# Optimization experiments

Measured on AMD Instinct MI355X. Metric: run time of the kernel, lower is better.

## Reference

```python
import jax, jax.numpy as jnp
import numpy as np

B, N, D, A = 2048, 32, 64, 8
MAX_ACTION = 1.0
VARIANCE = 1.0


def setup_inputs() -> dict:
    key = jax.random.key(0)
    k1, k2, k3, k4, k5 = jax.random.split(key, 5)
    mean = jax.random.normal(k1, (B, D), dtype=jnp.float32)
    # SPD covariance: small-scale L L^T + 0.1 I
    L = jax.random.normal(k2, (B, D, D), dtype=jnp.float32) * 0.05
    covariance = jnp.einsum('bij,bkj->bik', L, L) + 0.1 * jnp.eye(D, dtype=jnp.float32)
    centers = jax.random.normal(k3, (N, D), dtype=jnp.float32) * 0.5
    weights = jax.random.normal(k4, (N, A), dtype=jnp.float32) * 0.1
    lengthscales = jnp.ones((D,), dtype=jnp.float32) + 0.1 * jax.random.uniform(k5, (D,), dtype=jnp.float32)
    return {"mean": mean, "covariance": covariance, "centers": centers,
            "weights": weights, "lengthscales": lengthscales}


def squash_sin(mean, covariance, max_action):
    # mean: (B, K); covariance: (B, K, K)
    K = mean.shape[-1]
    ma = jnp.full((K,), max_action, dtype=mean.dtype)
    diag_cov = jnp.diagonal(covariance, axis1=-2, axis2=-1)          # (B, K)
    squashed_mean = ma * jnp.exp(-diag_cov / 2.0) * jnp.sin(mean)
    lq = -(diag_cov[..., :, None] + diag_cov[..., None, :]) / 2.0
    q = jnp.exp(lq)
    mean_diff = mean[..., :, None] - mean[..., None, :]
    mean_sum = mean[..., :, None] + mean[..., None, :]
    sq_cov = ((jnp.exp(lq + covariance) - q) * jnp.cos(mean_diff)
              - (jnp.exp(lq - covariance) - q) * jnp.cos(mean_sum))
    outer_max = ma[None, :] * ma[:, None]
    sq_cov = outer_max * sq_cov / 2.0
    # diag_embed of (B, K) -> (B, K, K)
    cross = (ma * jnp.exp(-diag_cov / 2.0) * jnp.cos(mean))[..., :, None] * jnp.eye(K, dtype=mean.dtype)
    return squashed_mean, sq_cov, cross


def reference(mean, covariance, centers, weights, lengthscales):
    b = mean.shape[0]
    inv_l = 1.0 / lengthscales                                        # (D,)
    # B_mat = diag(inv_l) @ cov @ diag(inv_l) + I  (B, D, D)
    B_mat = covariance * (inv_l[:, None] * inv_l[None, :]) + jnp.eye(D, dtype=mean.dtype)
    inp = centers[None, :, :] - mean[:, None, :]                      # (B, N, D)
    scaled_inp = inp * inv_l                                          # (B, N, D)
    t = jnp.swapaxes(jnp.linalg.solve(B_mat, jnp.swapaxes(scaled_inp, -1, -2)), -1, -2)  # (B, N, D)
    exp_term = jnp.exp(-0.5 * jnp.sum(scaled_inp * t, axis=-1))       # (B, N)
    _, log_det = jnp.linalg.slogdet(B_mat)                            # (B,)
    normalizer = VARIANCE * jnp.exp(-0.5 * log_det)
    phi_mean = normalizer[:, None] * exp_term                         # (B, N)
    action_mean = phi_mean @ weights                                  # (B, A)

    t_scaled = t * inv_l                                              # (B, N, D)
    cross_cov = jnp.einsum('bnd,bna->bda', t_scaled, phi_mean[..., None] * weights)  # (B, D, A)

    diff = centers[:, None, :] - centers[None, :, :]                  # (N, N, D)
    center_bar = (centers[:, None, :] + centers[None, :, :]) / 2.0    # (N, N, D)
    inv_lambda = 1.0 / lengthscales ** 2
    exp1 = -0.25 * jnp.sum(diff ** 2 * inv_lambda, axis=-1)           # (N, N)
    B_q = covariance + jnp.diag(lengthscales ** 2 / 2.0)[None]        # (B, D, D)
    z = center_bar[None] - mean[:, None, None, :]                     # (B, N, N, D)
    z_flat = z.reshape(b, N * N, D)
    solved = jnp.swapaxes(jnp.linalg.solve(B_q, jnp.swapaxes(z_flat, -1, -2)), -1, -2)
    exp2 = (-0.5 * jnp.sum(z_flat * solved, axis=-1)).reshape(b, N, N)
    log_det_lh = jnp.sum(jnp.log(lengthscales ** 2 / 2.0))
    _, log_det_bq = jnp.linalg.slogdet(B_q)
    c_q = jnp.exp(0.5 * (log_det_lh - log_det_bq))                    # (B,)
    Q = (VARIANCE ** 2) * c_q[:, None, None] * jnp.exp(exp1[None] + exp2)  # (B, N, N)

    action_cov = jnp.einsum('na,bnm,mc->bac', weights, Q, weights)    # (B, A, A)
    action_cov = action_cov - action_mean[:, :, None] * action_mean[:, None, :]
    action_cov = (action_cov + jnp.swapaxes(action_cov, -1, -2)) / 2.0
    action_cov = action_cov + jnp.eye(A, dtype=mean.dtype) * 1e-6

    action_mean, action_cov, C = squash_sin(action_mean, action_cov, MAX_ACTION)
    cross_cov = jnp.einsum('bda,bac->bdc', cross_cov, C)
    return (action_mean, action_cov, cross_cov)
```

## Files before the change

kernel.cpp:

```cpp
#include <hip/hip_runtime.h>
#include <math.h>


#define DD 64
#define NN 32
#define AA 8
#define NBATCH 2048
#define STR 68
#define W9 9

__global__ void rbf_prep(const float* __restrict__ centers,
                         const float* __restrict__ ls,
                         float* __restrict__ ws) {
    __shared__ float cen_s[NN * DD];
    __shared__ float il2_s[DD];
    int t = threadIdx.x;
    for (int e = t; e < NN * DD; e += 256) cen_s[e] = centers[e];
    if (t < DD) { float l = ls[t]; il2_s[t] = 1.0f / (l * l); }
    __syncthreads();
    int p = blockIdx.x * 256 + t;
    if (p < NN * NN) {
        int n = p >> 5, m = p & 31;
        float acc = 0.f;
        for (int d = 0; d < DD; ++d) {
            float df = cen_s[n * DD + d] - cen_s[m * DD + d];
            acc += df * df * il2_s[d];
        }
        ws[p] = -0.25f * acc;
    }
    if (blockIdx.x == 0 && t < DD) {
        float l = ls[t];
        float v = logf(0.5f * l * l);
        #pragma unroll
        for (int o = 1; o < 64; o <<= 1) v += __shfl_xor(v, o, 64);
        if (t == 0) ws[NN * NN] = v;
    }
}

__device__ __forceinline__ void factor_panel(float (&A)[4][4], const int p,
    float* __restrict__ LmT, float* __restrict__ diag_s, float* __restrict__ invd_s,
    const int lw)
{
    const int rb  = lw & 15;
    const int cbl = lw >> 4;
    const int c0  = 16 * p + 4 * cbl;
    const int r0  = 4 * rb;
    #pragma unroll
    for (int jj = 0; jj < 16; ++jj) {
        const int q  = jj >> 2;
        const int ci = jj & 3;
        const int j  = 16 * p + jj;
        const int fsrc = rb | (q << 4);
        const int hsrc = (4 * p + cbl) | (q << 4);
        const int dsrc = (4 * p + q) | (q << 4);
        float d  = __shfl(A[ci][ci], dsrc, 64);
        float f0 = __shfl(A[0][ci], fsrc, 64);
        float f1 = __shfl(A[1][ci], fsrc, 64);
        float f2 = __shfl(A[2][ci], fsrc, 64);
        float f3 = __shfl(A[3][ci], fsrc, 64);
        float h0 = __shfl(A[0][ci], hsrc, 64);
        float h1 = __shfl(A[1][ci], hsrc, 64);
        float h2 = __shfl(A[2][ci], hsrc, 64);
        float h3 = __shfl(A[3][ci], hsrc, 64);
        float id = __builtin_amdgcn_rcpf(d);
        float fr[4];
        fr[0] = (r0 + 0 > j) ? f0 : 0.f;
        fr[1] = (r0 + 1 > j) ? f1 : 0.f;
        fr[2] = (r0 + 2 > j) ? f2 : 0.f;
        fr[3] = (r0 + 3 > j) ? f3 : 0.f;
        float hc[4];
        hc[0] = (c0 + 0 > j) ? h0 * id : 0.f;
        hc[1] = (c0 + 1 > j) ? h1 * id : 0.f;
        hc[2] = (c0 + 2 > j) ? h2 * id : 0.f;
        hc[3] = (c0 + 3 > j) ? h3 * id : 0.f;
        #pragma unroll
        for (int s = 0; s < 4; ++s)
            #pragma unroll
            for (int c = 0; c < 4; ++c)
                A[s][c] -= fr[s] * hc[c];
        if (cbl == 0) {
            float4 v = make_float4(fr[0] * id, fr[1] * id, fr[2] * id, fr[3] * id);
            *(float4*)&LmT[j * STR + r0] = v;
        }
        if (lw == jj) { diag_s[j] = d; invd_s[j] = id; }
    }
}

__device__ __forceinline__ void trailing_one(float (&A)[4][4], const int p,
    const float* __restrict__ LmT, const float* __restrict__ diag_s,
    const int rb, const int cbX)
{
    #pragma unroll 2
    for (int kk = 0; kk < 16; ++kk) {
        const int k = 16 * p + kk;
        const float4 Lr = *(const float4*)&LmT[k * STR + 4 * rb];
        const float4 Lc = *(const float4*)&LmT[k * STR + 4 * cbX];
        const float dk = diag_s[k];
        const float h0 = Lc.x * dk, h1 = Lc.y * dk, h2 = Lc.z * dk, h3 = Lc.w * dk;
        A[0][0] -= Lr.x * h0; A[0][1] -= Lr.x * h1; A[0][2] -= Lr.x * h2; A[0][3] -= Lr.x * h3;
        A[1][0] -= Lr.y * h0; A[1][1] -= Lr.y * h1; A[1][2] -= Lr.y * h2; A[1][3] -= Lr.y * h3;
        A[2][0] -= Lr.z * h0; A[2][1] -= Lr.z * h1; A[2][2] -= Lr.z * h2; A[2][3] -= Lr.z * h3;
        A[3][0] -= Lr.w * h0; A[3][1] -= Lr.w * h1; A[3][2] -= Lr.w * h2; A[3][3] -= Lr.w * h3;
    }
}

__global__ __launch_bounds__(256, 3) void rbf_main(
    const float* __restrict__ mean,
    const float* __restrict__ cov,
    const float* __restrict__ centers,
    const float* __restrict__ weights,
    const float* __restrict__ ls,
    const float* __restrict__ ws,
    float* __restrict__ out)
{
    __shared__ __align__(16) float LmT1[DD * STR];
    __shared__ __align__(16) float LmT2[DD * STR];
    __shared__ __align__(16) float H_s[NN * STR];
    __shared__ __align__(16) float K_s[DD * W9];
    __shared__ __align__(16) float cp_s[DD * W9];
    __shared__ float diag1[DD], invd1[DD], diag2[DD], invd2[DD];
    __shared__ float mean_s[DD], invl_s[DD], l2h_s[DD];
    __shared__ float w9_s[NN * W9], phiw_s[NN * W9], U_s[NN * W9];
    __shared__ float am_s[AA], acr_s[AA * W9], Ca_s[AA];
    __shared__ float ldlh_s;

    const int t   = threadIdx.x;
    const int b   = blockIdx.x;
    const int lw  = t & 63;
    const int wv  = t >> 6;
    const int rb  = t & 15;
    const int cb  = t >> 4;
    const int cb1 = (cb + 8) & 15;
    const int wp1 = (wv + 2) & 3;
    const int grp = t >> 3;
    const int l8  = t & 7;
    const float* cvb = cov + (size_t)b * DD * DD;

    if (t < DD) {
        float l = ls[t];
        invl_s[t] = 1.0f / l;
        l2h_s[t]  = 0.5f * l * l;
        mean_s[t] = mean[(size_t)b * DD + t];
    }
    w9_s[(t >> 3) * W9 + (t & 7)] = weights[t];
    if (t == 0) ldlh_s = ws[NN * NN];
    __syncthreads();

    float A1[4][4], A2[4][4];
    {
        #pragma unroll
        for (int c = 0; c < 4; ++c) {
            const int gr = 4 * cb + c;
            const float4 cv = *(const float4*)(cvb + (size_t)gr * DD + 4 * rb);
            A2[0][c] = cv.x + ((4*rb+0 == gr) ? l2h_s[gr] : 0.0f);
            A2[1][c] = cv.y + ((4*rb+1 == gr) ? l2h_s[gr] : 0.0f);
            A2[2][c] = cv.z + ((4*rb+2 == gr) ? l2h_s[gr] : 0.0f);
            A2[3][c] = cv.w + ((4*rb+3 == gr) ? l2h_s[gr] : 0.0f);
        }
        const float il0 = invl_s[4*rb+0], il1 = invl_s[4*rb+1],
                    il2 = invl_s[4*rb+2], il3 = invl_s[4*rb+3];
        #pragma unroll
        for (int c = 0; c < 4; ++c) {
            const int gr = 4 * cb1 + c;
            const float4 cv = *(const float4*)(cvb + (size_t)gr * DD + 4 * rb);
            const float ilc = invl_s[gr];
            A1[0][c] = cv.x * il0 * ilc + ((4*rb+0 == gr) ? 1.0f : 0.0f);
            A1[1][c] = cv.y * il1 * ilc + ((4*rb+1 == gr) ? 1.0f : 0.0f);
            A1[2][c] = cv.z * il2 * ilc + ((4*rb+2 == gr) ? 1.0f : 0.0f);
            A1[3][c] = cv.w * il3 * ilc + ((4*rb+3 == gr) ? 1.0f : 0.0f);
        }
    }

    if (wv == 0) factor_panel(A2, 0, LmT2, diag2, invd2, lw);
    if (wv == 2) factor_panel(A1, 0, LmT1, diag1, invd1, lw);
    #pragma unroll 1
    for (int p = 0; p < 3; ++p) {
        __syncthreads();
        if (wv  >= p + 1) trailing_one(A2, p, LmT2, diag2, rb, cb);
        if (wp1 >= p + 1) trailing_one(A1, p, LmT1, diag1, rb, cb1);
        if (wv == p + 1)         factor_panel(A2, p + 1, LmT2, diag2, invd2, lw);
        if (wv == ((p + 3) & 3)) factor_panel(A1, p + 1, LmT1, diag1, invd1, lw);
    }
    __syncthreads();

    float logdet1, cq;
    {
        float v1 = logf(diag1[lw]);
        float v2 = logf(diag2[lw]);
        #pragma unroll
        for (int o = 1; o < 64; o <<= 1) {
            v1 += __shfl_xor(v1, o, 64);
            v2 += __shfl_xor(v2, o, 64);
        }
        logdet1 = v1;
        cq = expf(0.5f * (ldlh_s - v2));
    }

    {
        float x1[8], x2[8];
        const float4 ca  = *(const float4*)(centers + grp * DD + 8 * l8);
        const float4 cb4 = *(const float4*)(centers + grp * DD + 8 * l8 + 4);
        {
            float d0 = ca.x  - mean_s[8*l8+0], d1 = ca.y  - mean_s[8*l8+1];
            float d2 = ca.z  - mean_s[8*l8+2], d3 = ca.w  - mean_s[8*l8+3];
            float d4 = cb4.x - mean_s[8*l8+4], d5 = cb4.y - mean_s[8*l8+5];
            float d6 = cb4.z - mean_s[8*l8+6], d7 = cb4.w - mean_s[8*l8+7];
            x1[0] = d0 * invl_s[8*l8+0]; x2[0] = 0.5f * d0;
            x1[1] = d1 * invl_s[8*l8+1]; x2[1] = 0.5f * d1;
            x1[2] = d2 * invl_s[8*l8+2]; x2[2] = 0.5f * d2;
            x1[3] = d3 * invl_s[8*l8+3]; x2[3] = 0.5f * d3;
            x1[4] = d4 * invl_s[8*l8+4]; x2[4] = 0.5f * d4;
            x1[5] = d5 * invl_s[8*l8+5]; x2[5] = 0.5f * d5;
            x1[6] = d6 * invl_s[8*l8+6]; x2[6] = 0.5f * d6;
            x1[7] = d7 * invl_s[8*l8+7]; x2[7] = 0.5f * d7;
        }
        for (int k8 = 0; k8 < 8; ++k8) {
            #pragma unroll
            for (int kk = 0; kk < 8; ++kk) {
                const int k = 8 * k8 + kk;
                const int src = (lw & 56) | k8;
                float z1 = __shfl(x1[kk], src, 64);
                float z2 = __shfl(x2[kk], src, 64);
                #pragma unroll
                for (int s = 0; s < 8; ++s) {
                    x1[s] -= LmT1[k * STR + 8 * l8 + s] * z1;
                    x2[s] -= LmT2[k * STR + 8 * l8 + s] * z2;
                }
            }
        }
        float qf = 0.f;
        #pragma unroll
        for (int s = 0; s < 8; ++s) qf += x1[s] * x1[s] * invd1[8 * l8 + s];
        qf += __shfl_xor(qf, 1, 64);
        qf += __shfl_xor(qf, 2, 64);
        qf += __shfl_xor(qf, 4, 64);
        float ph = expf(-0.5f * (logdet1 + qf));
        phiw_s[grp * W9 + l8] = ph * w9_s[grp * W9 + l8];
        #pragma unroll
        for (int s = 0; s < 8; ++s)
            H_s[grp * STR + 8 * l8 + s] = x2[s] * sqrtf(invd2[8 * l8 + s]);
    }
    __syncthreads();

    if (t < 128) {
        const int d = t >> 1, a0 = (t & 1) * 4;
        const float md = mean_s[d], il = invl_s[d];
        float k0 = 0.f, k1 = 0.f, k2 = 0.f, k3 = 0.f;
        for (int n = 0; n < NN; ++n) {
            float sv = (centers[n * DD + d] - md) * il;
            k0 += sv * phiw_s[n * W9 + a0];
            k1 += sv * phiw_s[n * W9 + a0 + 1];
            k2 += sv * phiw_s[n * W9 + a0 + 2];
            k3 += sv * phiw_s[n * W9 + a0 + 3];
        }
        K_s[d * W9 + a0]     = k0;
        K_s[d * W9 + a0 + 1] = k1;
        K_s[d * W9 + a0 + 2] = k2;
        K_s[d * W9 + a0 + 3] = k3;
    } else if (t < 136) {
        int a = t - 128;
        float am = 0.f;
        for (int n = 0; n < NN; ++n) am += phiw_s[n * W9 + a];
        am_s[a] = am;
    }
    __syncthreads();

    if (wv == 0) {
        const int aa = t >> 3;
        float y[8];
        #pragma unroll
        for (int s = 0; s < 8; ++s) y[s] = K_s[(8 * l8 + s) * W9 + aa];
        for (int k8 = 0; k8 < 8; ++k8) {
            #pragma unroll
            for (int kk = 0; kk < 8; ++kk) {
                const int k = 8 * k8 + kk;
                float zk = __shfl(y[kk], (t & 56) | k8, 64);
                #pragma unroll
                for (int s = 0; s < 8; ++s)
                    y[s] -= LmT1[k * STR + 8 * l8 + s] * zk;
            }
        }
        #pragma unroll
        for (int s = 0; s < 8; ++s) y[s] *= invd1[8 * l8 + s];
        for (int i8 = 7; i8 >= 0; --i8) {
            #pragma unroll
            for (int ii = 7; ii >= 0; --ii) {
                const int i = 8 * i8 + ii;
                const float4 r0 = *(const float4*)&LmT1[i * STR + 8 * l8];
                const float4 r1 = *(const float4*)&LmT1[i * STR + 8 * l8 + 4];
                float part = r0.x*y[0] + r0.y*y[1] + r0.z*y[2] + r0.w*y[3]
                           + r1.x*y[4] + r1.y*y[5] + r1.z*y[6] + r1.w*y[7];
                part += __shfl_xor(part, 1, 64);
                part += __shfl_xor(part, 2, 64);
                part += __shfl_xor(part, 4, 64);
                if (l8 == i8) y[ii] -= part;
            }
        }
        #pragma unroll
        for (int s = 0; s < 8; ++s)
            cp_s[(8 * l8 + s) * W9 + aa] = y[s] * invl_s[8 * l8 + s];
    } else {
        const int g = (t - 64) >> 3;
        for (int n = g; n < NN; n += 24) {
            float acc[4] = {0.f, 0.f, 0.f, 0.f};
            const int rot = 2 * l8;
            #pragma unroll 2
            for (int e = 0; e < 16; ++e) {
                const int e4 = 4 * ((e + rot) & 15);
                const float4 hn = *(const float4*)&H_s[n * STR + e4];
                #pragma unroll
                for (int mm = 0; mm < 4; ++mm) {
                    const float4 hm = *(const float4*)&H_s[(4 * l8 + mm) * STR + e4];
                    float s0 = hn.x + hm.x, s1 = hn.y + hm.y;
                    float s2 = hn.z + hm.z, s3 = hn.w + hm.w;
                    acc[mm] += s0*s0 + s1*s1 + s2*s2 + s3*s3;
                }
            }
            const float4 e1 = *(const float4*)&ws[n * NN + 4 * l8];
            float Q0 = cq * expf(e1.x - 0.5f * acc[0]);
            float Q1 = cq * expf(e1.y - 0.5f * acc[1]);
            float Q2 = cq * expf(e1.z - 0.5f * acc[2]);
            float Q3 = cq * expf(e1.w - 0.5f * acc[3]);
            float u[8];
            #pragma unroll
            for (int a = 0; a < 8; ++a) {
                u[a] = Q0 * w9_s[(4*l8+0)*W9 + a] + Q1 * w9_s[(4*l8+1)*W9 + a]
                     + Q2 * w9_s[(4*l8+2)*W9 + a] + Q3 * w9_s[(4*l8+3)*W9 + a];
                u[a] += __shfl_xor(u[a], 1, 64);
                u[a] += __shfl_xor(u[a], 2, 64);
                u[a] += __shfl_xor(u[a], 4, 64);
            }
            float uv = (l8 == 0) ? u[0] : (l8 == 1) ? u[1] : (l8 == 2) ? u[2] : (l8 == 3) ? u[3]
                     : (l8 == 4) ? u[4] : (l8 == 5) ? u[5] : (l8 == 6) ? u[6] : u[7];
            U_s[n * W9 + l8] = uv;
        }
    }
    __syncthreads();

    if (t < 64) {
        const int a = t >> 3, c = t & 7;
        float acc2 = 0.f;
        for (int n = 0; n < NN; ++n) acc2 += w9_s[n * W9 + a] * U_s[n * W9 + c];
        acr_s[a * W9 + c] = acc2;
    }
    __syncthreads();

    float* out0 = out;
    float* out1 = out + (size_t)NBATCH * AA;
    float* out2 = out + (size_t)NBATCH * AA + (size_t)NBATCH * AA * AA;
    if (t < 64) {
        const int a = t >> 3, c = t & 7;
        const float ama = am_s[a], amc = am_s[c];
        const float vac = 0.5f * (acr_s[a * W9 + c] + acr_s[c * W9 + a])
                        - ama * amc + ((a == c) ? 1e-6f : 0.0f);
        const float dca = acr_s[a * W9 + a] - ama * ama + 1e-6f;
        const float dcc = acr_s[c * W9 + c] - amc * amc + 1e-6f;
        const float q = expf(-0.5f * (dca + dcc));
        const float sq = 0.5f * q * (expm1f(vac) * cosf(ama - amc)
                                   - expm1f(-vac) * cosf(ama + amc));
        out1[(size_t)b * 64 + t] = sq;
        if (t < AA) {
            float dct = acr_s[t * W9 + t] - am_s[t] * am_s[t] + 1e-6f;
            float e = expf(-0.5f * dct);
            out0[(size_t)b * AA + t] = e * sinf(am_s[t]);
            Ca_s[t] = e * cosf(am_s[t]);
        }
    }
    __syncthreads();
    #pragma unroll
    for (int e = 0; e < 2; ++e) {
        int idx = t + 256 * e;
        out2[(size_t)b * 512 + idx] = cp_s[(idx >> 3) * W9 + (idx & 7)] * Ca_s[idx & 7];
    }
}

extern "C" void kernel_launch(void* const* d_in, const int* in_sizes, int n_in,
                              void* d_out, int out_size, void* d_ws, size_t ws_size,
                              hipStream_t stream) {
    (void)in_sizes; (void)n_in; (void)out_size; (void)ws_size;
    const float* mean    = (const float*)d_in[0];
    const float* cov     = (const float*)d_in[1];
    const float* centers = (const float*)d_in[2];
    const float* weights = (const float*)d_in[3];
    const float* ls      = (const float*)d_in[4];
    float* ws = (float*)d_ws;
    float* o  = (float*)d_out;
    rbf_prep<<<4, 256, 0, stream>>>(centers, ls, ws);
    rbf_main<<<NBATCH, 256, 0, stream>>>(mean, cov, centers, weights, ls, ws, o);
}
```

Measured before the change: 218.4 us.

## Rebalance per-block work across waves and drop a barrier in rbf_main

```diff
diff --git a/kernel.cpp b/kernel.cpp
--- a/kernel.cpp
+++ b/kernel.cpp
@@ -118,9 +118,10 @@
     __shared__ __align__(16) float H_s[NN * STR];
     __shared__ __align__(16) float K_s[DD * W9];
     __shared__ __align__(16) float cp_s[DD * W9];
+    __shared__ __align__(16) float phiwc[NN * AA];
     __shared__ float diag1[DD], invd1[DD], diag2[DD], invd2[DD];
     __shared__ float mean_s[DD], invl_s[DD], l2h_s[DD];
-    __shared__ float w9_s[NN * W9], phiw_s[NN * W9], U_s[NN * W9];
+    __shared__ float w9_s[NN * W9], U_s[NN * W9];
     __shared__ float am_s[AA], acr_s[AA * W9], Ca_s[AA];
     __shared__ float ldlh_s;
 
@@ -132,7 +133,6 @@
     const int cb  = t >> 4;
     const int cb1 = (cb + 8) & 15;
     const int wp1 = (wv + 2) & 3;
-    const int grp = t >> 3;
     const int l8  = t & 7;
     const float* cvb = cov + (size_t)b * DD * DD;
 
@@ -196,77 +196,95 @@
         cq = expf(0.5f * (ldlh_s - v2));
     }
 
-    {
-        float x1[8], x2[8];
-        const float4 ca  = *(const float4*)(centers + grp * DD + 8 * l8);
-        const float4 cb4 = *(const float4*)(centers + grp * DD + 8 * l8 + 4);
+    if (wv < 2) {
+        const int gr8 = lw >> 3;
+        const int ra = 16 * wv + gr8;
+        const int rz = ra + 8;
+        float x1a[8], x2a[8], x1b[8], x2b[8];
         {
-            float d0 = ca.x  - mean_s[8*l8+0], d1 = ca.y  - mean_s[8*l8+1];
-            float d2 = ca.z  - mean_s[8*l8+2], d3 = ca.w  - mean_s[8*l8+3];
-            float d4 = cb4.x - mean_s[8*l8+4], d5 = cb4.y - mean_s[8*l8+5];
-            float d6 = cb4.z - mean_s[8*l8+6], d7 = cb4.w - mean_s[8*l8+7];
-            x1[0] = d0 * invl_s[8*l8+0]; x2[0] = 0.5f * d0;
-            x1[1] = d1 * invl_s[8*l8+1]; x2[1] = 0.5f * d1;
-            x1[2] = d2 * invl_s[8*l8+2]; x2[2] = 0.5f * d2;
-            x1[3] = d3 * invl_s[8*l8+3]; x2[3] = 0.5f * d3;
-            x1[4] = d4 * invl_s[8*l8+4]; x2[4] = 0.5f * d4;
-            x1[5] = d5 * invl_s[8*l8+5]; x2[5] = 0.5f * d5;
-            x1[6] = d6 * invl_s[8*l8+6]; x2[6] = 0.5f * d6;
-            x1[7] = d7 * invl_s[8*l8+7]; x2[7] = 0.5f * d7;
+            const float4 ca0 = *(const float4*)(centers + ra * DD + 8 * l8);
+            const float4 ca1 = *(const float4*)(centers + ra * DD + 8 * l8 + 4);
+            const float4 cb0 = *(const float4*)(centers + rz * DD + 8 * l8);
+            const float4 cb1v = *(const float4*)(centers + rz * DD + 8 * l8 + 4);
+            float da[8] = {ca0.x,ca0.y,ca0.z,ca0.w,ca1.x,ca1.y,ca1.z,ca1.w};
+            float db[8] = {cb0.x,cb0.y,cb0.z,cb0.w,cb1v.x,cb1v.y,cb1v.z,cb1v.w};
+            #pragma unroll
+            for (int s = 0; s < 8; ++s) {
+                const int i = 8 * l8 + s;
+                float d1 = da[s] - mean_s[i];
+                float d2 = db[s] - mean_s[i];
+                x1a[s] = d1 * invl_s[i]; x2a[s] = 0.5f * d1;
+                x1b[s] = d2 * invl_s[i]; x2b[s] = 0.5f * d2;
+            }
         }
         for (int k8 = 0; k8 < 8; ++k8) {
             #pragma unroll
             for (int kk = 0; kk < 8; ++kk) {
                 const int k = 8 * k8 + kk;
                 const int src = (lw & 56) | k8;
-                float z1 = __shfl(x1[kk], src, 64);
-                float z2 = __shfl(x2[kk], src, 64);
+                float z1a = __shfl(x1a[kk], src, 64);
+                float z1b = __shfl(x1b[kk], src, 64);
+                float z2a = __shfl(x2a[kk], src, 64);
+                float z2b = __shfl(x2b[kk], src, 64);
+                const float4 LA = *(const float4*)&LmT1[k * STR + 8 * l8];
+                const float4 LB = *(const float4*)&LmT1[k * STR + 8 * l8 + 4];
+                const float4 MA = *(const float4*)&LmT2[k * STR + 8 * l8];
+                const float4 MB = *(const float4*)&LmT2[k * STR + 8 * l8 + 4];
+                float l1[8] = {LA.x,LA.y,LA.z,LA.w,LB.x,LB.y,LB.z,LB.w};
+                float l2[8] = {MA.x,MA.y,MA.z,MA.w,MB.x,MB.y,MB.z,MB.w};
                 #pragma unroll
                 for (int s = 0; s < 8; ++s) {
-                    x1[s] -= LmT1[k * STR + 8 * l8 + s] * z1;
-                    x2[s] -= LmT2[k * STR + 8 * l8 + s] * z2;
+                    x1a[s] -= l1[s] * z1a;
+                    x1b[s] -= l1[s] * z1b;
+                    x2a[s] -= l2[s] * z2a;
+                    x2b[s] -= l2[s] * z2b;
                 }
             }
         }
-        float qf = 0.f;
-        #pragma unroll
-        for (int s = 0; s < 8; ++s) qf += x1[s] * x1[s] * invd1[8 * l8 + s];
-        qf += __shfl_xor(qf, 1, 64);
-        qf += __shfl_xor(qf, 2, 64);
-        qf += __shfl_xor(qf, 4, 64);
-        float ph = expf(-0.5f * (logdet1 + qf));
-        phiw_s[grp * W9 + l8] = ph * w9_s[grp * W9 + l8];
-        #pragma unroll
-        for (int s = 0; s < 8; ++s)
-            H_s[grp * STR + 8 * l8 + s] = x2[s] * sqrtf(invd2[8 * l8 + s]);
-    }
-    __syncthreads();
-
-    if (t < 128) {
-        const int d = t >> 1, a0 = (t & 1) * 4;
-        const float md = mean_s[d], il = invl_s[d];
-        float k0 = 0.f, k1 = 0.f, k2 = 0.f, k3 = 0.f;
-        for (int n = 0; n < NN; ++n) {
-            float sv = (centers[n * DD + d] - md) * il;
-            k0 += sv * phiw_s[n * W9 + a0];
-            k1 += sv * phiw_s[n * W9 + a0 + 1];
-            k2 += sv * phiw_s[n * W9 + a0 + 2];
-            k3 += sv * phiw_s[n * W9 + a0 + 3];
-        }
-        K_s[d * W9 + a0]     = k0;
-        K_s[d * W9 + a0 + 1] = k1;
-        K_s[d * W9 + a0 + 2] = k2;
-        K_s[d * W9 + a0 + 3] = k3;
-    } else if (t < 136) {
-        int a = t - 128;
-        float am = 0.f;
-        for (int n = 0; n < NN; ++n) am += phiw_s[n * W9 + a];
-        am_s[a] = am;
+        float qfa = 0.f, qfb = 0.f;
+        #pragma unroll
+        for (int s = 0; s < 8; ++s) {
+            qfa += x1a[s] * x1a[s] * invd1[8 * l8 + s];
+            qfb += x1b[s] * x1b[s] * invd1[8 * l8 + s];
+        }
+        qfa += __shfl_xor(qfa, 1, 64); qfa += __shfl_xor(qfa, 2, 64); qfa += __shfl_xor(qfa, 4, 64);
+        qfb += __shfl_xor(qfb, 1, 64); qfb += __shfl_xor(qfb, 2, 64); qfb += __shfl_xor(qfb, 4, 64);
+        float pha = expf(-0.5f * (logdet1 + qfa));
+        float phb = expf(-0.5f * (logdet1 + qfb));
+        phiwc[ra * AA + l8] = pha * w9_s[ra * W9 + l8];
+        phiwc[rz * AA + l8] = phb * w9_s[rz * W9 + l8];
+        {
+            float ha[8], hb[8];
+            #pragma unroll
+            for (int s = 0; s < 8; ++s) {
+                const float rs = sqrtf(invd2[8 * l8 + s]);
+                ha[s] = x2a[s] * rs;
+                hb[s] = x2b[s] * rs;
+            }
+            *(float4*)&H_s[ra * STR + 8 * l8]     = make_float4(ha[0],ha[1],ha[2],ha[3]);
+            *(float4*)&H_s[ra * STR + 8 * l8 + 4] = make_float4(ha[4],ha[5],ha[6],ha[7]);
+            *(float4*)&H_s[rz * STR + 8 * l8]     = make_float4(hb[0],hb[1],hb[2],hb[3]);
+            *(float4*)&H_s[rz * STR + 8 * l8 + 4] = make_float4(hb[4],hb[5],hb[6],hb[7]);
+        }
     }
     __syncthreads();
 
     if (wv == 0) {
-        const int aa = t >> 3;
+        {
+            const int d = lw;
+            const float md = mean_s[d], il = invl_s[d];
+            float k0=0.f,k1=0.f,k2=0.f,k3=0.f,k4=0.f,k5=0.f,k6=0.f,k7=0.f;
+            for (int n = 0; n < NN; ++n) {
+                const float sv = (centers[n * DD + d] - md) * il;
+                const float4 pa = *(const float4*)&phiwc[n * AA];
+                const float4 pb = *(const float4*)&phiwc[n * AA + 4];
+                k0 += sv * pa.x; k1 += sv * pa.y; k2 += sv * pa.z; k3 += sv * pa.w;
+                k4 += sv * pb.x; k5 += sv * pb.y; k6 += sv * pb.z; k7 += sv * pb.w;
+            }
+            K_s[d*W9+0]=k0; K_s[d*W9+1]=k1; K_s[d*W9+2]=k2; K_s[d*W9+3]=k3;
+            K_s[d*W9+4]=k4; K_s[d*W9+5]=k5; K_s[d*W9+6]=k6; K_s[d*W9+7]=k7;
+        }
+        const int aa = lw >> 3;
         float y[8];
         #pragma unroll
         for (int s = 0; s < 8; ++s) y[s] = K_s[(8 * l8 + s) * W9 + aa];
@@ -274,7 +292,7 @@
             #pragma unroll
             for (int kk = 0; kk < 8; ++kk) {
                 const int k = 8 * k8 + kk;
-                float zk = __shfl(y[kk], (t & 56) | k8, 64);
+                float zk = __shfl(y[kk], (lw & 56) | k8, 64);
                 #pragma unroll
                 for (int s = 0; s < 8; ++s)
                     y[s] -= LmT1[k * STR + 8 * l8 + s] * zk;
@@ -299,41 +317,68 @@
         #pragma unroll
         for (int s = 0; s < 8; ++s)
             cp_s[(8 * l8 + s) * W9 + aa] = y[s] * invl_s[8 * l8 + s];
+    } else if (wv == 3) {
+        if (lw < AA) {
+            const int a = lw;
+            float am = 0.f;
+            for (int n = 0; n < NN; ++n) am += phiwc[n * AA + a];
+            am_s[a] = am;
+        }
     } else {
-        const int g = (t - 64) >> 3;
-        for (int n = g; n < NN; n += 24) {
-            float acc[4] = {0.f, 0.f, 0.f, 0.f};
-            const int rot = 2 * l8;
-            #pragma unroll 2
-            for (int e = 0; e < 16; ++e) {
-                const int e4 = 4 * ((e + rot) & 15);
-                const float4 hn = *(const float4*)&H_s[n * STR + e4];
-                #pragma unroll
-                for (int mm = 0; mm < 4; ++mm) {
-                    const float4 hm = *(const float4*)&H_s[(4 * l8 + mm) * STR + e4];
-                    float s0 = hn.x + hm.x, s1 = hn.y + hm.y;
-                    float s2 = hn.z + hm.z, s3 = hn.w + hm.w;
-                    acc[mm] += s0*s0 + s1*s1 + s2*s2 + s3*s3;
+        const int g16 = (lw >> 3) + 8 * (wv - 1);
+        const int n0 = g16, n1 = g16 + 16;
+        float acc0[4] = {0.f,0.f,0.f,0.f}, acc1[4] = {0.f,0.f,0.f,0.f};
+        const int rot = 2 * l8;
+        #pragma unroll 2
+        for (int e = 0; e < 16; ++e) {
+            const int e4 = 4 * ((e + rot) & 15);
+            const float4 hn0 = *(const float4*)&H_s[n0 * STR + e4];
+            const float4 hn1 = *(const float4*)&H_s[n1 * STR + e4];
+            #pragma unroll
+            for (int mm = 0; mm < 4; ++mm) {
+                const float4 hm = *(const float4*)&H_s[(4 * l8 + mm) * STR + e4];
+                {
+                    float s0 = hn0.x + hm.x, s1 = hn0.y + hm.y;
+                    float s2 = hn0.z + hm.z, s3 = hn0.w + hm.w;
+                    acc0[mm] += s0*s0 + s1*s1 + s2*s2 + s3*s3;
                 }
-            }
-            const float4 e1 = *(const float4*)&ws[n * NN + 4 * l8];
-            float Q0 = cq * expf(e1.x - 0.5f * acc[0]);
-            float Q1 = cq * expf(e1.y - 0.5f * acc[1]);
-            float Q2 = cq * expf(e1.z - 0.5f * acc[2]);
-            float Q3 = cq * expf(e1.w - 0.5f * acc[3]);
-            float u[8];
-            #pragma unroll
-            for (int a = 0; a < 8; ++a) {
-                u[a] = Q0 * w9_s[(4*l8+0)*W9 + a] + Q1 * w9_s[(4*l8+1)*W9 + a]
-                     + Q2 * w9_s[(4*l8+2)*W9 + a] + Q3 * w9_s[(4*l8+3)*W9 + a];
-                u[a] += __shfl_xor(u[a], 1, 64);
-                u[a] += __shfl_xor(u[a], 2, 64);
-                u[a] += __shfl_xor(u[a], 4, 64);
-            }
-            float uv = (l8 == 0) ? u[0] : (l8 == 1) ? u[1] : (l8 == 2) ? u[2] : (l8 == 3) ? u[3]
-                     : (l8 == 4) ? u[4] : (l8 == 5) ? u[5] : (l8 == 6) ? u[6] : u[7];
-            U_s[n * W9 + l8] = uv;
-        }
+                {
+                    float s0 = hn1.x + hm.x, s1 = hn1.y + hm.y;
+                    float s2 = hn1.z + hm.z, s3 = hn1.w + hm.w;
+                    acc1[mm] += s0*s0 + s1*s1 + s2*s2 + s3*s3;
+                }
+            }
+        }
+        const float4 e1a = *(const float4*)&ws[n0 * NN + 4 * l8];
+        const float4 e1b = *(const float4*)&ws[n1 * NN + 4 * l8];
+        float Q0a = cq * expf(e1a.x - 0.5f * acc0[0]);
+        float Q1a = cq * expf(e1a.y - 0.5f * acc0[1]);
+        float Q2a = cq * expf(e1a.z - 0.5f * acc0[2]);
+        float Q3a = cq * expf(e1a.w - 0.5f * acc0[3]);
+        float Q0b = cq * expf(e1b.x - 0.5f * acc1[0]);
+        float Q1b = cq * expf(e1b.y - 0.5f * acc1[1]);
+        float Q2b = cq * expf(e1b.z - 0.5f * acc1[2]);
+        float Q3b = cq * expf(e1b.w - 0.5f * acc1[3]);
+        float ua[8], ub[8];
+        #pragma unroll
+        for (int a = 0; a < 8; ++a) {
+            const float w0 = w9_s[(4*l8+0)*W9 + a], w1 = w9_s[(4*l8+1)*W9 + a];
+            const float w2 = w9_s[(4*l8+2)*W9 + a], w3 = w9_s[(4*l8+3)*W9 + a];
+            ua[a] = Q0a*w0 + Q1a*w1 + Q2a*w2 + Q3a*w3;
+            ub[a] = Q0b*w0 + Q1b*w1 + Q2b*w2 + Q3b*w3;
+            ua[a] += __shfl_xor(ua[a], 1, 64);
+            ua[a] += __shfl_xor(ua[a], 2, 64);
+            ua[a] += __shfl_xor(ua[a], 4, 64);
+            ub[a] += __shfl_xor(ub[a], 1, 64);
+            ub[a] += __shfl_xor(ub[a], 2, 64);
+            ub[a] += __shfl_xor(ub[a], 4, 64);
+        }
+        float uva = (l8 == 0) ? ua[0] : (l8 == 1) ? ua[1] : (l8 == 2) ? ua[2] : (l8 == 3) ? ua[3]
+                  : (l8 == 4) ? ua[4] : (l8 == 5) ? ua[5] : (l8 == 6) ? ua[6] : ua[7];
+        float uvb = (l8 == 0) ? ub[0] : (l8 == 1) ? ub[1] : (l8 == 2) ? ub[2] : (l8 == 3) ? ub[3]
+                  : (l8 == 4) ? ub[4] : (l8 == 5) ? ub[5] : (l8 == 6) ? ub[6] : ub[7];
+        U_s[n0 * W9 + l8] = uva;
+        U_s[n1 * W9 + l8] = uvb;
     }
     __syncthreads();
 
```

New measurement: 217.6 us. About the same (-0.4%).
